# Kernel optimization log

Measured on AMD Instinct MI355X. Metric: run time of the kernel, lower is better.

Reference implementation:

```python
import jax, jax.numpy as jnp
import numpy as np

B, T, HID, OUT = 32, 2048, 1024, 1024
DV = 1024
NEG_INF = jnp.float32(-jnp.inf)


def setup_inputs() -> dict:
    key = jax.random.key(0)
    ks = jax.random.split(key, 10)
    hidden = jax.random.normal(ks[0], (B, HID), dtype=jnp.float32)
    enc_key = jax.random.normal(ks[1], (B, T, OUT), dtype=jnp.float32)
    value = jax.random.normal(ks[2], (B, T, DV), dtype=jnp.float32)
    seq_lens = jnp.maximum(jax.random.randint(ks[3], (B,), 0, T), 1).astype(jnp.int32)
    # learned parameters (PyTorch Linear: y = x @ W.T + b; we store W already transposed)
    s_q = 1.0 / np.sqrt(HID)
    s_1 = 1.0 / np.sqrt(OUT)
    s_2 = 1.0 / np.sqrt(OUT // 2)
    Wq = jax.random.uniform(ks[4], (HID, OUT), minval=-s_q, maxval=s_q, dtype=jnp.float32)
    bq = jax.random.uniform(ks[5], (OUT,), minval=-s_q, maxval=s_q, dtype=jnp.float32)
    W1 = jax.random.uniform(ks[6], (OUT, OUT // 2), minval=-s_1, maxval=s_1, dtype=jnp.float32)
    b1 = jax.random.uniform(ks[7], (OUT // 2,), minval=-s_1, maxval=s_1, dtype=jnp.float32)
    W2 = jax.random.uniform(ks[8], (OUT // 2, 1), minval=-s_2, maxval=s_2, dtype=jnp.float32)
    b2 = jax.random.uniform(ks[9], (1,), minval=-s_2, maxval=s_2, dtype=jnp.float32)
    return {"hidden": hidden, "key": enc_key, "value": value, "seq_lens": seq_lens,
            "Wq": Wq, "bq": bq, "W1": W1, "b1": b1, "W2": W2, "b2": b2}


def reference(hidden, key, value, seq_lens, Wq, bq, W1, b1, W2, b2):
    # query projection: [B, OUT]
    query = hidden @ Wq + bq
    # additive Bahdanau: tanh(key + query) -> [B, T, OUT]
    h = jnp.tanh(key + query[:, None, :])
    # 2-layer score MLP (dropout p=0.2 is identity in eval mode)
    h = h @ W1 + b1                      # [B, T, OUT//2]
    scores = (h @ W2 + b2)[..., 0]       # [B, T]
    # mask positions >= seq_len with -inf, then softmax over T
    pos = jnp.arange(scores.shape[1])
    scores = jnp.where(pos[None, :] < seq_lens[:, None], scores, NEG_INF)
    attn = jax.nn.softmax(scores, axis=-1)  # [B, T]
    # context = attn @ value -> [B, DV]
    context = jnp.einsum('bt,btd->bd', attn, value)
    return (context, attn)
```

## Files before the change

kernel.cpp:

```cpp
#include <hip/hip_runtime.h>
#include <math.h>

#define BB 32
#define TT 2048
#define DD 1024
#define HF 512

#define QKS 64
#define QCH (DD / QKS)

#define CHK 32
#define NCH (TT / CHK)

#define KSC 2.88539008177792681f

#if __has_builtin(__builtin_amdgcn_exp2f)
#define EXP2F(x) __builtin_amdgcn_exp2f(x)
#else
#define EXP2F(x) exp2f(x)
#endif

__global__ void __launch_bounds__(256) prep_query_kernel(
        const float* __restrict__ hidden, const float* __restrict__ Wq,
        const float* __restrict__ W1, const float* __restrict__ b1,
        const float* __restrict__ W2, const float* __restrict__ b2,
        float* __restrict__ w, float* __restrict__ cbias,
        float* __restrict__ qpart) {
    __shared__ float smem[BB * QCH];
    int bx  = blockIdx.x;
    int tid = threadIdx.x;

    if (bx < 4) {
        int d = bx * 256 + tid;
        const float* row = W1 + (size_t)d * HF;
        float acc = 0.0f;
        #pragma unroll 8
        for (int j = 0; j < HF; j += 4) {
            float4 a = *(const float4*)(row + j);
            float4 b = *(const float4*)(W2 + j);
            acc += a.x * b.x + a.y * b.y + a.z * b.z + a.w * b.w;
        }
        w[d] = acc;
        return;
    }
    if (bx == 4) {
        __shared__ float red[256];
        float s = b1[tid] * W2[tid] + b1[tid + 256] * W2[tid + 256];
        red[tid] = s;
        __syncthreads();
        for (int off = 128; off; off >>= 1) {
            if (tid < off) red[tid] += red[tid + off];
            __syncthreads();
        }
        if (tid == 0) cbias[0] = red[0] + b2[0];
        return;
    }
    int idx = bx - 5, otile = idx & 3, ks = idx >> 2;
    int o = otile * 256 + tid, h0 = ks * QCH;
    if (tid < 128) {
        int r = tid >> 2, c4 = (tid & 3) << 2;
        *(float4*)&smem[r * QCH + c4] = *(const float4*)&hidden[(size_t)r * DD + h0 + c4];
    }
    __syncthreads();

    float wv[QCH];
    #pragma unroll
    for (int h = 0; h < QCH; ++h)
        wv[h] = Wq[(size_t)(h0 + h) * DD + o];

    float acc[BB];
    #pragma unroll
    for (int b = 0; b < BB; ++b) acc[b] = 0.0f;
    #pragma unroll
    for (int h = 0; h < QCH; ++h) {
        #pragma unroll
        for (int b = 0; b < BB; ++b)
            acc[b] = fmaf(smem[b * QCH + h], wv[h], acc[b]);
    }
    #pragma unroll
    for (int b = 0; b < BB; ++b)
        qpart[((size_t)ks * BB + b) * DD + o] = acc[b];
}

__global__ void __launch_bounds__(256) qreduce_kernel(
        const float* __restrict__ qpart, const float* __restrict__ bq,
        const float* __restrict__ w, float* __restrict__ cb,
        float* __restrict__ query) {
    __shared__ float part[256];
    int bx = blockIdx.x, tid = threadIdx.x;
    if (bx == 256) {
        float s = w[tid] + w[tid + 256] + w[tid + 512] + w[tid + 768];
        part[tid] = s;
        __syncthreads();
        for (int off = 128; off; off >>= 1) {
            if (tid < off) part[tid] += part[tid + off];
            __syncthreads();
        }
        if (tid == 0) cb[1] = cb[0] + part[0];
        return;
    }
    int e = tid & 127, g = tid >> 7;
    int i = bx * 128 + e;
    int ks0 = g * (QKS / 2);
    float a0 = 0.0f, a1 = 0.0f, a2 = 0.0f, a3 = 0.0f;
    #pragma unroll 8
    for (int k = 0; k < QKS / 2; k += 4) {
        size_t base = (size_t)(ks0 + k) * (BB * DD) + i;
        a0 += qpart[base];
        a1 += qpart[base + (size_t)(BB * DD)];
        a2 += qpart[base + 2 * (size_t)(BB * DD)];
        a3 += qpart[base + 3 * (size_t)(BB * DD)];
    }
    part[tid] = (a0 + a1) + (a2 + a3);
    __syncthreads();
    if (g == 0) query[i] = bq[i & (DD - 1)] + part[tid] + part[tid + 128];
}

__global__ void __launch_bounds__(256, 6) score_ctx_kernel(
        const float* __restrict__ key, const float* __restrict__ value,
        const float* __restrict__ query, const float* __restrict__ w,
        const float* __restrict__ cb, const int* __restrict__ seq_lens,
        float* __restrict__ escore, float* __restrict__ psum,
        float* __restrict__ partial) {
    int item = blockIdx.x;
    int b    = item & (BB - 1);
    int x    = item >> 5;
    int len  = seq_lens[b];
    int t0   = x * CHK;
    if (t0 >= len) return;

    __shared__ float wsh[DD];
    __shared__ float qsh[DD];
    __shared__ float esm[CHK];
    int tid = threadIdx.x;
    { int i4 = tid * 4;
      float4 w4 = *(const float4*)&w[i4];
      float4 q4 = *(const float4*)&query[(size_t)b * DD + i4];
      float4 ws = {-2.0f * w4.x, -2.0f * w4.y, -2.0f * w4.z, -2.0f * w4.w};
      float4 qs = {KSC * q4.x, KSC * q4.y, KSC * q4.z, KSC * q4.w};
      *(float4*)&wsh[i4] = ws;
      *(float4*)&qsh[i4] = qs; }
    __syncthreads();

    int wave = tid >> 6, lane = tid & 63;
    float c2 = cb[1];
    const float* kb0 = key + (size_t)b * TT * DD;

    float4 kreg[2][4];
    {
        const float* kr = kb0 + (size_t)(t0 + wave) * DD;
        #pragma unroll
        for (int s = 0; s < 4; ++s)
            kreg[0][s] = *(const float4*)(kr + s * 256 + lane * 4);
    }
    #pragma unroll
    for (int j = 0; j < 8; ++j) {
        if (j < 7) {
            const float* kr = kb0 + (size_t)(t0 + (j + 1) * 4 + wave) * DD;
            #pragma unroll
            for (int s = 0; s < 4; ++s)
                kreg[(j + 1) & 1][s] = *(const float4*)(kr + s * 256 + lane * 4);
        }
        float acc = 0.0f;
        #pragma unroll
        for (int s = 0; s < 4; ++s) {
            int d = s * 256 + lane * 4;
            float4 kv = kreg[j & 1][s];
            float4 qv = *(const float4*)&qsh[d];
            float4 wv = *(const float4*)&wsh[d];
            float r0 = __builtin_amdgcn_rcpf(EXP2F(fmaf(kv.x, KSC, qv.x)) + 1.0f);
            float r1 = __builtin_amdgcn_rcpf(EXP2F(fmaf(kv.y, KSC, qv.y)) + 1.0f);
            float r2 = __builtin_amdgcn_rcpf(EXP2F(fmaf(kv.z, KSC, qv.z)) + 1.0f);
            float r3 = __builtin_amdgcn_rcpf(EXP2F(fmaf(kv.w, KSC, qv.w)) + 1.0f);
            acc = fmaf(wv.x, r0, acc);
            acc = fmaf(wv.y, r1, acc);
            acc = fmaf(wv.z, r2, acc);
            acc = fmaf(wv.w, r3, acc);
        }
        #pragma unroll
        for (int off = 32; off; off >>= 1) acc += __shfl_down(acc, off);
        if (lane == 0) {
            int t = t0 + j * 4 + wave;
            esm[j * 4 + wave] = (t < len) ? __expf(acc + c2) : 0.0f;
        }
    }
    __syncthreads();

    if (tid < CHK) escore[(size_t)b * TT + t0 + tid] = esm[tid];
    if (tid == 0) {
        float s = 0.0f;
        #pragma unroll
        for (int i = 0; i < CHK; ++i) s += esm[i];
        psum[b * NCH + x] = s;
    }

    int d4 = tid * 4;
    const float* vbase = value + (size_t)b * TT * DD + d4;
    float4 A0 = {0.0f, 0.0f, 0.0f, 0.0f};
    float4 A1 = A0, A2 = A0, A3 = A0;
    #pragma unroll 2
    for (int tt = 0; tt < CHK; tt += 4) {
        float e0 = esm[tt], e1 = esm[tt + 1], e2 = esm[tt + 2], e3 = esm[tt + 3];
        float4 v0 = *(const float4*)(vbase + (size_t)(t0 + tt    ) * DD);
        float4 v1 = *(const float4*)(vbase + (size_t)(t0 + tt + 1) * DD);
        float4 v2 = *(const float4*)(vbase + (size_t)(t0 + tt + 2) * DD);
        float4 v3 = *(const float4*)(vbase + (size_t)(t0 + tt + 3) * DD);
        A0.x = fmaf(e0, v0.x, A0.x); A0.y = fmaf(e0, v0.y, A0.y);
        A0.z = fmaf(e0, v0.z, A0.z); A0.w = fmaf(e0, v0.w, A0.w);
        A1.x = fmaf(e1, v1.x, A1.x); A1.y = fmaf(e1, v1.y, A1.y);
        A1.z = fmaf(e1, v1.z, A1.z); A1.w = fmaf(e1, v1.w, A1.w);
        A2.x = fmaf(e2, v2.x, A2.x); A2.y = fmaf(e2, v2.y, A2.y);
        A2.z = fmaf(e2, v2.z, A2.z); A2.w = fmaf(e2, v2.w, A2.w);
        A3.x = fmaf(e3, v3.x, A3.x); A3.y = fmaf(e3, v3.y, A3.y);
        A3.z = fmaf(e3, v3.z, A3.z); A3.w = fmaf(e3, v3.w, A3.w);
    }
    float4 R;
    R.x = (A0.x + A1.x) + (A2.x + A3.x);
    R.y = (A0.y + A1.y) + (A2.y + A3.y);
    R.z = (A0.z + A1.z) + (A2.z + A3.z);
    R.w = (A0.w + A1.w) + (A2.w + A3.w);
    *(float4*)&partial[((size_t)(b * NCH + x)) * DD + d4] = R;
}

__global__ void __launch_bounds__(256) finalize_kernel(
        const float* __restrict__ partial, const float* __restrict__ escore,
        const float* __restrict__ psum, const int* __restrict__ seq_lens,
        float* __restrict__ ctx, float* __restrict__ attn) {
    __shared__ float red[NCH];
    __shared__ float part[256];
    int bx = blockIdx.x, tid = threadIdx.x;
    int b  = (bx < 256) ? (bx >> 3) : ((bx - 256) >> 1);
    int len = seq_lens[b];
    int nch = (len + CHK - 1) / CHK;

    if (tid < NCH) red[tid] = (tid < nch) ? psum[b * NCH + tid] : 0.0f;
    __syncthreads();
    #pragma unroll
    for (int off = NCH / 2; off; off >>= 1) {
        if (tid < off) red[tid] += red[tid + off];
        __syncthreads();
    }
    float Sinv = 1.0f / red[0];

    if (bx < 256) {
        int e = tid & 127, g = tid >> 7;
        int d = (bx & 7) * 128 + e;
        const float* pb = partial + (size_t)b * NCH * DD + d;
        int cbeg = g * 32, cend = min(nch, cbeg + 32);
        float a0 = 0.0f, a1 = 0.0f, a2 = 0.0f, a3 = 0.0f;
        int c = cbeg;
        for (; c + 3 < cend; c += 4) {
            a0 += pb[(size_t)(c + 0) * DD];
            a1 += pb[(size_t)(c + 1) * DD];
            a2 += pb[(size_t)(c + 2) * DD];
            a3 += pb[(size_t)(c + 3) * DD];
        }
        for (; c < cend; ++c) a0 += pb[(size_t)c * DD];
        part[tid] = (a0 + a1) + (a2 + a3);
        __syncthreads();
        if (g == 0) ctx[(size_t)b * DD + d] = (part[tid] + part[tid + 128]) * Sinv;
    } else {
        int idx = (bx - 256) * 1024 + tid * 4;
        int t   = idx & (TT - 1);
        float4 e4 = *(const float4*)&escore[(size_t)b * TT + t];
        float4 o;
        o.x = (t + 0 < len) ? e4.x * Sinv : 0.0f;
        o.y = (t + 1 < len) ? e4.y * Sinv : 0.0f;
        o.z = (t + 2 < len) ? e4.z * Sinv : 0.0f;
        o.w = (t + 3 < len) ? e4.w * Sinv : 0.0f;
        *(float4*)&attn[(size_t)b * TT + t] = o;
    }
}

extern "C" void kernel_launch(void* const* d_in, const int* in_sizes, int n_in,
                              void* d_out, int out_size, void* d_ws, size_t ws_size,
                              hipStream_t stream) {
    const float* hidden   = (const float*)d_in[0];
    const float* key      = (const float*)d_in[1];
    const float* value    = (const float*)d_in[2];
    const int*   seq_lens = (const int*)  d_in[3];
    const float* Wq       = (const float*)d_in[4];
    const float* bq       = (const float*)d_in[5];
    const float* W1       = (const float*)d_in[6];
    const float* b1       = (const float*)d_in[7];
    const float* W2       = (const float*)d_in[8];
    const float* b2       = (const float*)d_in[9];

    float* out  = (float*)d_out;
    float* ctx  = out;
    float* attn = out + BB * DD;

    float* ws      = (float*)d_ws;
    float* w       = ws;
    float* cb      = ws + 1024;
    float* query   = ws + 2048;
    float* qpart   = query + BB * DD;
    float* escore  = qpart + (size_t)QKS * BB * DD;
    float* psum    = escore + BB * TT;
    float* partial = psum + BB * NCH;

    prep_query_kernel<<<dim3(5 + 4 * QKS), dim3(256), 0, stream>>>(
        hidden, Wq, W1, b1, W2, b2, w, cb, qpart);
    qreduce_kernel<<<dim3(BB * DD / 128 + 1), dim3(256), 0, stream>>>(
        qpart, bq, w, cb, query);
    score_ctx_kernel<<<dim3(BB * NCH), dim3(256), 0, stream>>>(
        key, value, query, w, cb, seq_lens, escore, psum, partial);
    finalize_kernel<<<dim3(320), dim3(256), 0, stream>>>(
        partial, escore, psum, seq_lens, ctx, attn);
}
```

Baseline: 85.54 us.

## Fuse score and context per wave, keep weights in registers, double chunk

Restructures the score/context kernel so each wave computes a row's score and immediately accumulates the value row weighted by it. Query and weight vectors now live in registers, which removes the shared-memory staging, the block barrier and the separate value pass. The chunk size doubles to 64, and each wave writes its own partial context and partial sum. Finalize now reduces four times as many partial rows per chunk, which adds partial-buffer traffic and register pressure (launch bounds lowered to 4).

New measurement: 165.7 us. 1.94x slower.

```diff
diff --git a/kernel.cpp b/kernel.cpp
--- a/kernel.cpp
+++ b/kernel.cpp
@@ -9,7 +9,7 @@
 #define QKS 64
 #define QCH (DD / QKS)
 
-#define CHK 32
+#define CHK 64
 #define NCH (TT / CHK)
 
 #define KSC 2.88539008177792681f
@@ -116,7 +116,7 @@
     if (g == 0) query[i] = bq[i & (DD - 1)] + part[tid] + part[tid + 128];
 }
 
-__global__ void __launch_bounds__(256, 6) score_ctx_kernel(
+__global__ void __launch_bounds__(256, 4) stream_kernel(
         const float* __restrict__ key, const float* __restrict__ value,
         const float* __restrict__ query, const float* __restrict__ w,
         const float* __restrict__ cb, const int* __restrict__ seq_lens,
@@ -129,114 +129,110 @@
     int t0   = x * CHK;
     if (t0 >= len) return;
 
-    __shared__ float wsh[DD];
-    __shared__ float qsh[DD];
-    __shared__ float esm[CHK];
-    int tid = threadIdx.x;
-    { int i4 = tid * 4;
-      float4 w4 = *(const float4*)&w[i4];
-      float4 q4 = *(const float4*)&query[(size_t)b * DD + i4];
-      float4 ws = {-2.0f * w4.x, -2.0f * w4.y, -2.0f * w4.z, -2.0f * w4.w};
-      float4 qs = {KSC * q4.x, KSC * q4.y, KSC * q4.z, KSC * q4.w};
-      *(float4*)&wsh[i4] = ws;
-      *(float4*)&qsh[i4] = qs; }
-    __syncthreads();
-
+    int tid  = threadIdx.x;
     int wave = tid >> 6, lane = tid & 63;
     float c2 = cb[1];
-    const float* kb0 = key + (size_t)b * TT * DD;
+    int l4 = lane * 4;
+
+    float4 wv[4], qv[4];
+    {
+        const float* qb = query + (size_t)b * DD;
+        #pragma unroll
+        for (int s = 0; s < 4; ++s) {
+            float4 w4 = *(const float4*)(w + s * 256 + l4);
+            float4 q4 = *(const float4*)(qb + s * 256 + l4);
+            wv[s] = make_float4(-2.0f * w4.x, -2.0f * w4.y, -2.0f * w4.z, -2.0f * w4.w);
+            qv[s] = make_float4(KSC * q4.x, KSC * q4.y, KSC * q4.z, KSC * q4.w);
+        }
+    }
+
+    const float* kb0 = key   + (size_t)b * TT * DD;
+    const float* vb0 = value + (size_t)b * TT * DD;
+
+    float4 acc[4];
+    #pragma unroll
+    for (int s = 0; s < 4; ++s) acc[s] = make_float4(0.f, 0.f, 0.f, 0.f);
+    float esum = 0.0f;
 
     float4 kreg[2][4];
     {
         const float* kr = kb0 + (size_t)(t0 + wave) * DD;
         #pragma unroll
         for (int s = 0; s < 4; ++s)
-            kreg[0][s] = *(const float4*)(kr + s * 256 + lane * 4);
-    }
-    #pragma unroll
-    for (int j = 0; j < 8; ++j) {
-        if (j < 7) {
-            const float* kr = kb0 + (size_t)(t0 + (j + 1) * 4 + wave) * DD;
+            kreg[0][s] = *(const float4*)(kr + s * 256 + l4);
+    }
+
+    #pragma unroll
+    for (int j = 0; j < CHK / 4; ++j) {
+        int t = t0 + j * 4 + wave;
+        if (j < CHK / 4 - 1) {
+            const float* kr = kb0 + (size_t)(t + 4) * DD;
             #pragma unroll
             for (int s = 0; s < 4; ++s)
-                kreg[(j + 1) & 1][s] = *(const float4*)(kr + s * 256 + lane * 4);
-        }
-        float acc = 0.0f;
+                kreg[(j + 1) & 1][s] = *(const float4*)(kr + s * 256 + l4);
+        }
+        const float* vr = vb0 + (size_t)t * DD;
+        float4 v0 = *(const float4*)(vr + l4);
+        float4 v1 = *(const float4*)(vr + 256 + l4);
+        float4 v2 = *(const float4*)(vr + 512 + l4);
+        float4 v3 = *(const float4*)(vr + 768 + l4);
+
+        float sa = 0.0f;
         #pragma unroll
         for (int s = 0; s < 4; ++s) {
-            int d = s * 256 + lane * 4;
             float4 kv = kreg[j & 1][s];
-            float4 qv = *(const float4*)&qsh[d];
-            float4 wv = *(const float4*)&wsh[d];
-            float r0 = __builtin_amdgcn_rcpf(EXP2F(fmaf(kv.x, KSC, qv.x)) + 1.0f);
-            float r1 = __builtin_amdgcn_rcpf(EXP2F(fmaf(kv.y, KSC, qv.y)) + 1.0f);
-            float r2 = __builtin_amdgcn_rcpf(EXP2F(fmaf(kv.z, KSC, qv.z)) + 1.0f);
-            float r3 = __builtin_amdgcn_rcpf(EXP2F(fmaf(kv.w, KSC, qv.w)) + 1.0f);
-            acc = fmaf(wv.x, r0, acc);
-            acc = fmaf(wv.y, r1, acc);
-            acc = fmaf(wv.z, r2, acc);
-            acc = fmaf(wv.w, r3, acc);
-        }
-        #pragma unroll
-        for (int off = 32; off; off >>= 1) acc += __shfl_down(acc, off);
-        if (lane == 0) {
-            int t = t0 + j * 4 + wave;
-            esm[j * 4 + wave] = (t < len) ? __expf(acc + c2) : 0.0f;
-        }
-    }
-    __syncthreads();
-
-    if (tid < CHK) escore[(size_t)b * TT + t0 + tid] = esm[tid];
-    if (tid == 0) {
-        float s = 0.0f;
-        #pragma unroll
-        for (int i = 0; i < CHK; ++i) s += esm[i];
-        psum[b * NCH + x] = s;
-    }
-
-    int d4 = tid * 4;
-    const float* vbase = value + (size_t)b * TT * DD + d4;
-    float4 A0 = {0.0f, 0.0f, 0.0f, 0.0f};
-    float4 A1 = A0, A2 = A0, A3 = A0;
-    #pragma unroll 2
-    for (int tt = 0; tt < CHK; tt += 4) {
-        float e0 = esm[tt], e1 = esm[tt + 1], e2 = esm[tt + 2], e3 = esm[tt + 3];
-        float4 v0 = *(const float4*)(vbase + (size_t)(t0 + tt    ) * DD);
-        float4 v1 = *(const float4*)(vbase + (size_t)(t0 + tt + 1) * DD);
-        float4 v2 = *(const float4*)(vbase + (size_t)(t0 + tt + 2) * DD);
-        float4 v3 = *(const float4*)(vbase + (size_t)(t0 + tt + 3) * DD);
-        A0.x = fmaf(e0, v0.x, A0.x); A0.y = fmaf(e0, v0.y, A0.y);
-        A0.z = fmaf(e0, v0.z, A0.z); A0.w = fmaf(e0, v0.w, A0.w);
-        A1.x = fmaf(e1, v1.x, A1.x); A1.y = fmaf(e1, v1.y, A1.y);
-        A1.z = fmaf(e1, v1.z, A1.z); A1.w = fmaf(e1, v1.w, A1.w);
-        A2.x = fmaf(e2, v2.x, A2.x); A2.y = fmaf(e2, v2.y, A2.y);
-        A2.z = fmaf(e2, v2.z, A2.z); A2.w = fmaf(e2, v2.w, A2.w);
-        A3.x = fmaf(e3, v3.x, A3.x); A3.y = fmaf(e3, v3.y, A3.y);
-        A3.z = fmaf(e3, v3.z, A3.z); A3.w = fmaf(e3, v3.w, A3.w);
-    }
-    float4 R;
-    R.x = (A0.x + A1.x) + (A2.x + A3.x);
-    R.y = (A0.y + A1.y) + (A2.y + A3.y);
-    R.z = (A0.z + A1.z) + (A2.z + A3.z);
-    R.w = (A0.w + A1.w) + (A2.w + A3.w);
-    *(float4*)&partial[((size_t)(b * NCH + x)) * DD + d4] = R;
+            float r0 = __builtin_amdgcn_rcpf(EXP2F(fmaf(kv.x, KSC, qv[s].x)) + 1.0f);
+            float r1 = __builtin_amdgcn_rcpf(EXP2F(fmaf(kv.y, KSC, qv[s].y)) + 1.0f);
+            float r2 = __builtin_amdgcn_rcpf(EXP2F(fmaf(kv.z, KSC, qv[s].z)) + 1.0f);
+            float r3 = __builtin_amdgcn_rcpf(EXP2F(fmaf(kv.w, KSC, qv[s].w)) + 1.0f);
+            sa = fmaf(wv[s].x, r0, sa);
+            sa = fmaf(wv[s].y, r1, sa);
+            sa = fmaf(wv[s].z, r2, sa);
+            sa = fmaf(wv[s].w, r3, sa);
+        }
+        #pragma unroll
+        for (int m = 1; m < 64; m <<= 1) sa += __shfl_xor(sa, m);
+
+        float e = (t < len) ? __expf(sa + c2) : 0.0f;
+        esum += e;
+        if (lane == 0) escore[(size_t)b * TT + t] = e;
+
+        acc[0].x = fmaf(e, v0.x, acc[0].x); acc[0].y = fmaf(e, v0.y, acc[0].y);
+        acc[0].z = fmaf(e, v0.z, acc[0].z); acc[0].w = fmaf(e, v0.w, acc[0].w);
+        acc[1].x = fmaf(e, v1.x, acc[1].x); acc[1].y = fmaf(e, v1.y, acc[1].y);
+        acc[1].z = fmaf(e, v1.z, acc[1].z); acc[1].w = fmaf(e, v1.w, acc[1].w);
+        acc[2].x = fmaf(e, v2.x, acc[2].x); acc[2].y = fmaf(e, v2.y, acc[2].y);
+        acc[2].z = fmaf(e, v2.z, acc[2].z); acc[2].w = fmaf(e, v2.w, acc[2].w);
+        acc[3].x = fmaf(e, v3.x, acc[3].x); acc[3].y = fmaf(e, v3.y, acc[3].y);
+        acc[3].z = fmaf(e, v3.z, acc[3].z); acc[3].w = fmaf(e, v3.w, acc[3].w);
+    }
+
+    size_t pbase = (((size_t)(b * NCH + x)) * 4 + wave) * DD + l4;
+    #pragma unroll
+    for (int s = 0; s < 4; ++s)
+        *(float4*)&partial[pbase + s * 256] = acc[s];
+    if (lane == 0) psum[((b * NCH + x) << 2) + wave] = esum;
 }
 
 __global__ void __launch_bounds__(256) finalize_kernel(
         const float* __restrict__ partial, const float* __restrict__ escore,
         const float* __restrict__ psum, const int* __restrict__ seq_lens,
         float* __restrict__ ctx, float* __restrict__ attn) {
-    __shared__ float red[NCH];
+    __shared__ float red[128];
     __shared__ float part[256];
     int bx = blockIdx.x, tid = threadIdx.x;
     int b  = (bx < 256) ? (bx >> 3) : ((bx - 256) >> 1);
     int len = seq_lens[b];
     int nch = (len + CHK - 1) / CHK;
-
-    if (tid < NCH) red[tid] = (tid < nch) ? psum[b * NCH + tid] : 0.0f;
+    int nterms = nch * 4;
+
+    if (tid < 128) {
+        int c = tid >> 2, wv_ = tid & 3;
+        red[tid] = (c < nch) ? psum[((b * NCH + c) << 2) + wv_] : 0.0f;
+    }
     __syncthreads();
     #pragma unroll
-    for (int off = NCH / 2; off; off >>= 1) {
+    for (int off = 64; off; off >>= 1) {
         if (tid < off) red[tid] += red[tid + off];
         __syncthreads();
     }
@@ -245,17 +241,18 @@
     if (bx < 256) {
         int e = tid & 127, g = tid >> 7;
         int d = (bx & 7) * 128 + e;
-        const float* pb = partial + (size_t)b * NCH * DD + d;
-        int cbeg = g * 32, cend = min(nch, cbeg + 32);
+        const float* pb = partial + (size_t)(b * NCH * 4) * DD + d;
+        int half = nterms >> 1;
+        int mbeg = g * half, mend = mbeg + half;
         float a0 = 0.0f, a1 = 0.0f, a2 = 0.0f, a3 = 0.0f;
-        int c = cbeg;
-        for (; c + 3 < cend; c += 4) {
-            a0 += pb[(size_t)(c + 0) * DD];
-            a1 += pb[(size_t)(c + 1) * DD];
-            a2 += pb[(size_t)(c + 2) * DD];
-            a3 += pb[(size_t)(c + 3) * DD];
-        }
-        for (; c < cend; ++c) a0 += pb[(size_t)c * DD];
+        int m = mbeg;
+        for (; m + 3 < mend; m += 4) {
+            a0 += pb[(size_t)(m + 0) * DD];
+            a1 += pb[(size_t)(m + 1) * DD];
+            a2 += pb[(size_t)(m + 2) * DD];
+            a3 += pb[(size_t)(m + 3) * DD];
+        }
+        for (; m < mend; ++m) a0 += pb[(size_t)m * DD];
         part[tid] = (a0 + a1) + (a2 + a3);
         __syncthreads();
         if (g == 0) ctx[(size_t)b * DD + d] = (part[tid] + part[tid + 128]) * Sinv;
@@ -297,13 +294,13 @@
     float* qpart   = query + BB * DD;
     float* escore  = qpart + (size_t)QKS * BB * DD;
     float* psum    = escore + BB * TT;
-    float* partial = psum + BB * NCH;
+    float* partial = psum + BB * NCH * 4;
 
     prep_query_kernel<<<dim3(5 + 4 * QKS), dim3(256), 0, stream>>>(
         hidden, Wq, W1, b1, W2, b2, w, cb, qpart);
     qreduce_kernel<<<dim3(BB * DD / 128 + 1), dim3(256), 0, stream>>>(
         qpart, bq, w, cb, query);
-    score_ctx_kernel<<<dim3(BB * NCH), dim3(256), 0, stream>>>(
+    stream_kernel<<<dim3(BB * NCH), dim3(256), 0, stream>>>(
         key, value, query, w, cb, seq_lens, escore, psum, partial);
     finalize_kernel<<<dim3(320), dim3(256), 0, stream>>>(
         partial, escore, psum, seq_lens, ctx, attn);
```
